# Kernel optimization log

Measured on AMD Instinct MI355X. Metric: run time of the kernel, lower is better.

## Reference

```python
import jax, jax.numpy as jnp
import numpy as np

B, S = 32, 2048
DIM_ACTION = 32
DIM_STRUCT = 64
HIDDEN = 128  # mlp_hidden_dim default = dim_action * 4
EPS = 1e-12   # F.normalize eps


def l2norm(t):
    n = jnp.linalg.norm(t, axis=-1, keepdims=True)
    return t / jnp.maximum(n, EPS)


def setup_inputs() -> dict:
    key = jax.random.key(0)
    ks = jax.random.split(key, 9)
    sd = lambda fan_in: 1.0 / np.sqrt(fan_in)
    inp = {
        "actions": jax.random.normal(ks[0], (B, S, DIM_ACTION), dtype=jnp.float32),
        # MLP: dim_action -> hidden -> hidden -> dim_structure^2 (depth=2 hidden relu layers)
        "w0": jax.random.uniform(ks[1], (DIM_ACTION, HIDDEN), jnp.float32, -sd(DIM_ACTION), sd(DIM_ACTION)),
        "b0": jnp.zeros((HIDDEN,), jnp.float32),
        "w1": jax.random.uniform(ks[2], (HIDDEN, HIDDEN), jnp.float32, -sd(HIDDEN), sd(HIDDEN)),
        "b1": jnp.zeros((HIDDEN,), jnp.float32),
        "w2": jax.random.uniform(ks[3], (HIDDEN, DIM_STRUCT * DIM_STRUCT), jnp.float32, -sd(HIDDEN), sd(HIDDEN)),
        "b2": jnp.zeros((DIM_STRUCT * DIM_STRUCT,), jnp.float32),
        # RNN init hidden parameter [1, dim_structure], ~N(0, 0.01)
        "init_hidden": jax.random.normal(ks[4], (1, DIM_STRUCT), dtype=jnp.float32) * 0.01,
    }
    return inp


def reference(actions, w0, b0, w1, b1, w2, b2, init_hidden):
    # MLP to transitions: [B, S, d*d]
    h = jax.nn.relu(jnp.einsum("bsa,ah->bsh", actions, w0) + b0)
    h = jax.nn.relu(jnp.einsum("bsh,hk->bsk", h, w1) + b1)
    t = jnp.einsum("bsh,ho->bso", h, w2) + b2
    transitions = t.reshape(B, S, DIM_STRUCT, DIM_STRUCT)  # [B, S, i, j]

    # RNN: hidden_{t+1} = l2norm(relu(hidden_t @ T_t)), scanned over seq
    hidden0 = jnp.broadcast_to(l2norm(init_hidden), (B, DIM_STRUCT))

    def step(hidden, trans):  # trans: [B, i, j]
        hidden = jnp.einsum("bi,bij->bj", hidden, trans)
        hidden = l2norm(jax.nn.relu(hidden))
        return hidden, hidden

    trans_seq = jnp.swapaxes(transitions, 0, 1)  # [S, B, i, j]
    _, hiddens = jax.lax.scan(step, hidden0, trans_seq)  # [S, B, d]
    return jnp.swapaxes(hiddens, 0, 1)  # [B, S, d]
```

## Files before the change

### kernel.cpp

```cpp
#include <hip/hip_runtime.h>

#define B_ 32
#define S_ 2048
#define DA 32
#define DH 128
#define DS 64
#define DS2 4096

typedef _Float16 half8 __attribute__((ext_vector_type(8)));
typedef float f32x4 __attribute__((ext_vector_type(4)));

template <int CTRL>
__device__ __forceinline__ float dpp_add(float x) {
  int t = __builtin_amdgcn_update_dpp(0, __float_as_int(x), CTRL, 0xF, 0xF, true);
  return x + __int_as_float(t);
}
__device__ __forceinline__ float row_sum16(float x) {
  x = dpp_add<0xB1>(x);
  x = dpp_add<0x4E>(x);
  x = dpp_add<0x141>(x);
  x = dpp_add<0x140>(x);
  return x;
}

__device__ __forceinline__ void gl2lds16(const void* g, void* l) {
  __builtin_amdgcn_global_load_lds(
      (const __attribute__((address_space(1))) void*)g,
      (__attribute__((address_space(3))) void*)l, 16, 0, 0);
}

struct SharedRnn {
  float4 ring[6][16][64];
  int flags[6];
  int cons;
};
struct SharedGemm {
  _Float16 Ah[128 * 128];
  _Float16 Al[128 * 128];
  _Float16 Bh[128 * 128];
  _Float16 Bl[128 * 128];
};
struct SharedMlp {
  float a_t[DA][64];
  float w0_l[DA][DH];
  float h0t[DH][64];
};
union SharedU {
  SharedRnn r;
  SharedGemm g;
  SharedMlp m;
};

__global__ __launch_bounds__(256) void k_split(
    const float* __restrict__ w2, _Float16* __restrict__ w2h,
    _Float16* __restrict__ w2l)
{
  for (int e = blockIdx.x * 256 + threadIdx.x; e < DH * DS2;
       e += gridDim.x * 256) {
    int n = e >> 7, k = e & 127;
    float v = w2[(size_t)k * DS2 + n];
    _Float16 hi = (_Float16)v;
    _Float16 lo = (_Float16)((v - (float)hi) * 2048.0f);
    int kk = k ^ ((n & 7) << 3);
    w2h[(size_t)n * DH + kk] = hi;
    w2l[(size_t)n * DH + kk] = lo;
  }
}

__device__ __forceinline__ void mlp_tile(
    const float* __restrict__ actions, const float* __restrict__ w0,
    const float* __restrict__ b0, const float* __restrict__ w1,
    const float* __restrict__ b1, _Float16* __restrict__ h1h,
    _Float16* __restrict__ h1l, int s_base, int m0, SharedMlp& sm, int tid)
{
#pragma unroll
  for (int q = 0; q < 2; ++q) {
    int g = tid + 256 * q;
    int tok = g >> 3, kq = g & 7;
    int tl = m0 + tok;
    int b = tl & 31, s = s_base + (tl >> 5);
    float4 v = *(const float4*)(actions + ((size_t)b * S_ + s) * DA + 4 * kq);
    sm.a_t[4 * kq + 0][tok] = v.x; sm.a_t[4 * kq + 1][tok] = v.y;
    sm.a_t[4 * kq + 2][tok] = v.z; sm.a_t[4 * kq + 3][tok] = v.w;
  }
#pragma unroll
  for (int q = 0; q < 4; ++q) {
    int g = tid + 256 * q;
    ((float4*)&sm.w0_l[0][0])[g] = ((const float4*)w0)[g];
  }
  __syncthreads();

  const int tm = tid & 15;
  const int tn = tid >> 4;

  float acc[4][8];
#pragma unroll
  for (int mi = 0; mi < 4; ++mi)
#pragma unroll
    for (int ni = 0; ni < 8; ++ni) acc[mi][ni] = 0.f;

#pragma unroll 4
  for (int k = 0; k < DA; ++k) {
    float4 a4 = *(const float4*)&sm.a_t[k][4 * tm];
    float4 wa = *(const float4*)&sm.w0_l[k][8 * tn];
    float4 wb = *(const float4*)&sm.w0_l[k][8 * tn + 4];
    float av[4] = {a4.x, a4.y, a4.z, a4.w};
    float wv[8] = {wa.x, wa.y, wa.z, wa.w, wb.x, wb.y, wb.z, wb.w};
#pragma unroll
    for (int mi = 0; mi < 4; ++mi)
#pragma unroll
      for (int ni = 0; ni < 8; ++ni) acc[mi][ni] += av[mi] * wv[ni];
  }
  {
    float4 ba = *(const float4*)(b0 + 8 * tn);
    float4 bb = *(const float4*)(b0 + 8 * tn + 4);
    float bv[8] = {ba.x, ba.y, ba.z, ba.w, bb.x, bb.y, bb.z, bb.w};
#pragma unroll
    for (int mi = 0; mi < 4; ++mi)
#pragma unroll
      for (int ni = 0; ni < 8; ++ni)
        sm.h0t[8 * tn + ni][4 * tm + mi] = fmaxf(acc[mi][ni] + bv[ni], 0.f);
  }
  __syncthreads();

  float acc1[4][8];
#pragma unroll
  for (int mi = 0; mi < 4; ++mi)
#pragma unroll
    for (int ni = 0; ni < 8; ++ni) acc1[mi][ni] = 0.f;

#pragma unroll 4
  for (int k = 0; k < DH; ++k) {
    float4 h4 = *(const float4*)&sm.h0t[k][4 * tm];
    float4 wa = *(const float4*)(w1 + (size_t)k * DH + 8 * tn);
    float4 wb = *(const float4*)(w1 + (size_t)k * DH + 8 * tn + 4);
    float av[4] = {h4.x, h4.y, h4.z, h4.w};
    float wv[8] = {wa.x, wa.y, wa.z, wa.w, wb.x, wb.y, wb.z, wb.w};
#pragma unroll
    for (int mi = 0; mi < 4; ++mi)
#pragma unroll
      for (int ni = 0; ni < 8; ++ni) acc1[mi][ni] += av[mi] * wv[ni];
  }
  {
    float4 ba = *(const float4*)(b1 + 8 * tn);
    float4 bb = *(const float4*)(b1 + 8 * tn + 4);
    float bv[8] = {ba.x, ba.y, ba.z, ba.w, bb.x, bb.y, bb.z, bb.w};
#pragma unroll
    for (int mi = 0; mi < 4; ++mi) {
      const int m = m0 + 4 * tm + mi;
      half8 hv, lv;
#pragma unroll
      for (int ni = 0; ni < 8; ++ni) {
        float h = fmaxf(acc1[mi][ni] + bv[ni], 0.f);
        _Float16 hi = (_Float16)h;
        hv[ni] = hi;
        lv[ni] = (_Float16)((h - (float)hi) * 2048.0f);
      }
      const int off = m * DH + ((8 * tn) ^ ((m & 7) << 3));
      *(half8*)(h1h + off) = hv;
      *(half8*)(h1l + off) = lv;
    }
  }
}

__device__ __forceinline__ void trans_loop(
    const _Float16* __restrict__ h1h, const _Float16* __restrict__ h1l,
    const _Float16* __restrict__ w2h, const _Float16* __restrict__ w2l,
    const float* __restrict__ b2, float* __restrict__ trans,
    int MT, int x, SharedGemm& sg, int tid)
{
  const int w  = tid >> 6;
  const int lw = tid & 63;
  const int strip = x / 7;
  const int idx   = x % 7;
  const int n0 = strip * 128;

  auto stage32k = [&](const _Float16* src, _Float16* dst) {
    const _Float16* s = src + w * 4096 + lw * 8;
    _Float16* d = dst + w * 4096;
#pragma unroll
    for (int i = 0; i < 8; ++i)
      gl2lds16(s + i * 512, d + i * 512);
  };

  stage32k(w2h + (size_t)n0 * DH, sg.Bh);
  stage32k(w2l + (size_t)n0 * DH, sg.Bl);

  const int fr = lw & 15;
  const int kg = lw >> 4;
  const int wr = w >> 1, wc = w & 1;

  float b2v[4];
#pragma unroll
  for (int fn = 0; fn < 4; ++fn)
    b2v[fn] = b2[n0 + wc * 64 + fn * 16 + fr];

  const f32x4 fz = {0.f, 0.f, 0.f, 0.f};

  for (int mt = idx; mt < MT; mt += 7) {
    const int m0 = mt * 128;
    stage32k(h1h + (size_t)m0 * DH, sg.Ah);
    stage32k(h1l + (size_t)m0 * DH, sg.Al);
    asm volatile("s_waitcnt vmcnt(0)" ::: "memory");
    __syncthreads();

    f32x4 ahh[4][4], axx[4][4], all_[4][4];
#pragma unroll
    for (int fm = 0; fm < 4; ++fm)
#pragma unroll
      for (int fn = 0; fn < 4; ++fn) {
        ahh[fm][fn] = fz;
        axx[fm][fn] = fz;
        all_[fm][fn] = fz;
      }

#pragma unroll
    for (int kc = 0; kc < 4; ++kc) {
      const int k0 = kc * 32 + kg * 8;
      half8 bh[4], bl[4];
#pragma unroll
      for (int fn = 0; fn < 4; ++fn) {
        const int n = wc * 64 + fn * 16 + fr;
        const int off = n * DH + (k0 ^ ((n & 7) << 3));
        bh[fn] = *(const half8*)&sg.Bh[off];
        bl[fn] = *(const half8*)&sg.Bl[off];
      }
#pragma unroll
      for (int fm = 0; fm < 4; ++fm) {
        const int m = wr * 64 + fm * 16 + fr;
        const int off = m * DH + (k0 ^ ((m & 7) << 3));
        half8 ah = *(const half8*)&sg.Ah[off];
        half8 al = *(const half8*)&sg.Al[off];
#pragma unroll
        for (int fn = 0; fn < 4; ++fn) {
          ahh[fm][fn] = __builtin_amdgcn_mfma_f32_16x16x32_f16(
              ah, bh[fn], ahh[fm][fn], 0, 0, 0);
          axx[fm][fn] = __builtin_amdgcn_mfma_f32_16x16x32_f16(
              ah, bl[fn], axx[fm][fn], 0, 0, 0);
          axx[fm][fn] = __builtin_amdgcn_mfma_f32_16x16x32_f16(
              al, bh[fn], axx[fm][fn], 0, 0, 0);
          all_[fm][fn] = __builtin_amdgcn_mfma_f32_16x16x32_f16(
              al, bl[fn], all_[fm][fn], 0, 0, 0);
        }
      }
    }
    __syncthreads();

#pragma unroll
    for (int fm = 0; fm < 4; ++fm) {
#pragma unroll
      for (int fn = 0; fn < 4; ++fn) {
        const int col = n0 + wc * 64 + fn * 16 + fr;
        float* dst = trans +
            (size_t)(m0 + wr * 64 + fm * 16 + kg * 4) * DS2 + col;
#pragma unroll
        for (int r = 0; r < 4; ++r) {
          float v = ahh[fm][fn][r] + axx[fm][fn][r] * (1.0f / 2048.0f) +
                    all_[fm][fn][r] * (1.0f / 4194304.0f) + b2v[fn];
          dst[(size_t)r * DS2] = v;
        }
      }
    }
  }
}

__global__ __launch_bounds__(256) void k_mlp01(
    const float* __restrict__ actions, const float* __restrict__ w0,
    const float* __restrict__ b0, const float* __restrict__ w1,
    const float* __restrict__ b1, _Float16* __restrict__ h1h,
    _Float16* __restrict__ h1l, int s_base)
{
  __shared__ SharedMlp sm;
  mlp_tile(actions, w0, b0, w1, b1, h1h, h1l, s_base, blockIdx.x * 64, sm,
           threadIdx.x);
}

__global__ __launch_bounds__(256, 1) void k_comb(
    const float* __restrict__ actions, const float* __restrict__ w0,
    const float* __restrict__ b0, const float* __restrict__ w1,
    const float* __restrict__ b1, const _Float16* __restrict__ w2h,
    const _Float16* __restrict__ w2l, const float* __restrict__ b2,
    const float* __restrict__ init_hidden,
    float* __restrict__ trans0, float* __restrict__ trans1,
    _Float16* __restrict__ h1h0, _Float16* __restrict__ h1l0,
    _Float16* __restrict__ h1h1, _Float16* __restrict__ h1l1,
    float* __restrict__ hstate, float* __restrict__ out,
    int c, int SC, int nch)
{
  __shared__ SharedU sh;
  const int tid = threadIdx.x;
  const int M = SC * 32;

  if (blockIdx.x >= 32) {
    const int x = blockIdx.x - 32;
    if (c < nch) {
      const _Float16* h1h = (c & 1) ? h1h1 : h1h0;
      const _Float16* h1l = (c & 1) ? h1l1 : h1l0;
      float* trans = (c & 1) ? trans1 : trans0;
      trans_loop(h1h, h1l, w2h, w2l, b2, trans, M / 128, x, sh.g, tid);
      if (c + 1 < nch) {
        __syncthreads();
        _Float16* hh = ((c + 1) & 1) ? h1h1 : h1h0;
        _Float16* hl = ((c + 1) & 1) ? h1l1 : h1l0;
        for (int j = x; j < M / 64; j += 224) {
          mlp_tile(actions, w0, b0, w1, b1, hh, hl, (c + 1) * SC, j * 64,
                   sh.m, tid);
          __syncthreads();
        }
      }
    }
    return;
  }

  if (c == 0) return;
  const int cc = c - 1;
  const float* trans = (cc & 1) ? trans1 : trans0;
  const int s_base = cc * SC;
  const int wv = tid >> 6;
  const int lane = tid & 63;
  const int b = blockIdx.x;

  if (tid < 6) sh.r.flags[tid] = 0;
  if (tid == 6) sh.r.cons = 0;
  __syncthreads();

  const float* base = trans + (size_t)b * DS2;

  if (wv > 0) {
    const int p = wv - 1;
    int prev = -1;
    for (int s = p; s < SC; s += 3) {
      while (s - __hip_atomic_load(&sh.r.cons, __ATOMIC_RELAXED,
                                   __HIP_MEMORY_SCOPE_WORKGROUP) > 5)
        __builtin_amdgcn_s_sleep(2);
      const int slot = s % 6;
      const float* g = base + (size_t)s * (32 * DS2) + 4 * lane;
      float* l = (float*)&sh.r.ring[slot][0][0];
#pragma unroll
      for (int q = 0; q < 16; ++q)
        gl2lds16(g + q * 256, l + q * 256);
      if (prev >= 0) {
        asm volatile("s_waitcnt vmcnt(16)" ::: "memory");
        __hip_atomic_store(&sh.r.flags[prev % 6], prev + 1, __ATOMIC_RELAXED,
                           __HIP_MEMORY_SCOPE_WORKGROUP);
      }
      prev = s;
    }
    if (prev >= 0) {
      asm volatile("s_waitcnt vmcnt(0)" ::: "memory");
      __hip_atomic_store(&sh.r.flags[prev % 6], prev + 1, __ATOMIC_RELAXED,
                         __HIP_MEMORY_SCOPE_WORKGROUP);
    }
  } else {
    const int d = lane >> 4;
    const int cq = lane & 15;
    const bool d1 = (d & 1), d2 = (d & 2);
    const int pb = lane & 48;

    float4 hq;
    if (cc == 0) {
      hq = *(const float4*)(init_hidden + 4 * cq);
      float ss0 = row_sum16(hq.x * hq.x + hq.y * hq.y + hq.z * hq.z + hq.w * hq.w);
      float iv0 = 1.0f / fmaxf(sqrtf(ss0), 1e-12f);
      hq.x *= iv0; hq.y *= iv0; hq.z *= iv0; hq.w *= iv0;
    } else {
      hq = *(const float4*)(hstate + b * DS + 4 * cq);
    }
    float inv_prev = 1.0f;

    float* outp = out + ((size_t)b * S_ + s_base) * DS + 4 * cq;
    int fpre = -1;
    for (int s = 0; s < SC; ++s) {
      const int slot = s % 6;
      if (fpre < s + 1) {
        while (__hip_atomic_load(&sh.r.flags[slot], __ATOMIC_ACQUIRE,
                                 __HIP_MEMORY_SCOPE_WORKGROUP) < s + 1)
          __builtin_amdgcn_s_sleep(0);
      }
      fpre = __hip_atomic_load(&sh.r.flags[(s + 1) % 6], __ATOMIC_ACQUIRE,
                               __HIP_MEMORY_SCOPE_WORKGROUP);

      float hsel = d2 ? (d1 ? hq.w : hq.z) : (d1 ? hq.y : hq.x);
      float ax = 0.f, ay = 0.f, az = 0.f, aw = 0.f;
#pragma unroll
      for (int q = 0; q < 16; ++q) {
        float4 t4 = sh.r.ring[slot][q][lane];
        float hb = __shfl(hsel, pb + q, 64);
        ax += hb * t4.x; ay += hb * t4.y;
        az += hb * t4.z; aw += hb * t4.w;
      }
      __hip_atomic_store(&sh.r.cons, s + 1, __ATOMIC_RELAXED,
                         __HIP_MEMORY_SCOPE_WORKGROUP);

      ax += __shfl_xor(ax, 16, 64); ax += __shfl_xor(ax, 32, 64);
      ay += __shfl_xor(ay, 16, 64); ay += __shfl_xor(ay, 32, 64);
      az += __shfl_xor(az, 16, 64); az += __shfl_xor(az, 32, 64);
      aw += __shfl_xor(aw, 16, 64); aw += __shfl_xor(aw, 32, 64);
      hq.x = fmaxf(ax * inv_prev, 0.f);
      hq.y = fmaxf(ay * inv_prev, 0.f);
      hq.z = fmaxf(az * inv_prev, 0.f);
      hq.w = fmaxf(aw * inv_prev, 0.f);
      float ss = row_sum16(hq.x * hq.x + hq.y * hq.y + hq.z * hq.z + hq.w * hq.w);
      float inv = 1.0f / fmaxf(sqrtf(ss), 1e-12f);
      if (d == 0) {
        float4 o;
        o.x = hq.x * inv; o.y = hq.y * inv; o.z = hq.z * inv; o.w = hq.w * inv;
        *(float4*)(outp + (size_t)s * DS) = o;
      }
      inv_prev = inv;
    }
    if (d == 0) {
      float4 o;
      o.x = hq.x * inv_prev; o.y = hq.y * inv_prev;
      o.z = hq.z * inv_prev; o.w = hq.w * inv_prev;
      *(float4*)(hstate + b * DS + 4 * cq) = o;
    }
  }
}

extern "C" void kernel_launch(void* const* d_in, const int* in_sizes, int n_in,
                              void* d_out, int out_size, void* d_ws, size_t ws_size,
                              hipStream_t stream) {
  const float* actions     = (const float*)d_in[0];
  const float* w0          = (const float*)d_in[1];
  const float* b0          = (const float*)d_in[2];
  const float* w1          = (const float*)d_in[3];
  const float* b1          = (const float*)d_in[4];
  const float* w2          = (const float*)d_in[5];
  const float* b2          = (const float*)d_in[6];
  const float* init_hidden = (const float*)d_in[7];
  float* out = (float*)d_out;

  int SC = 2048;
  while (SC > 4) {
    size_t need = 2 * (size_t)SC * 32 * DS2 * 4
                + 4 * (size_t)SC * 32 * DH * 2
                + 2 * (size_t)DH * DS2 * 2
                + (size_t)B_ * DS * 4;
    if (need <= ws_size) break;
    SC >>= 1;
  }
  char* p = (char*)d_ws;
  float* trans0 = (float*)p;        p += (size_t)SC * 32 * DS2 * 4;
  float* trans1 = (float*)p;        p += (size_t)SC * 32 * DS2 * 4;
  _Float16* h1h0 = (_Float16*)p;    p += (size_t)SC * 32 * DH * 2;
  _Float16* h1l0 = (_Float16*)p;    p += (size_t)SC * 32 * DH * 2;
  _Float16* h1h1 = (_Float16*)p;    p += (size_t)SC * 32 * DH * 2;
  _Float16* h1l1 = (_Float16*)p;    p += (size_t)SC * 32 * DH * 2;
  _Float16* w2h  = (_Float16*)p;    p += (size_t)DH * DS2 * 2;
  _Float16* w2l  = (_Float16*)p;    p += (size_t)DH * DS2 * 2;
  float* hstate  = (float*)p;

  const int M = SC * 32;
  const int nch = S_ / SC;

  hipLaunchKernelGGL(k_split, dim3(512), dim3(256), 0, stream, w2, w2h, w2l);
  hipLaunchKernelGGL(k_mlp01, dim3(M / 64), dim3(256), 0, stream,
                     actions, w0, b0, w1, b1, h1h0, h1l0, 0);
  for (int c = 0; c <= nch; ++c) {
    hipLaunchKernelGGL(k_comb, dim3(256), dim3(256), 0, stream,
                       actions, w0, b0, w1, b1, w2h, w2l, b2, init_hidden,
                       trans0, trans1, h1h0, h1l0, h1h1, h1l1, hstate, out,
                       c, SC, nch);
  }
}
```

Measured before the change: 1.584 ms.

## Store transition matrices as fp16 plus e4m3 residual to cut memory traffic

```diff
diff --git a/kernel.cpp b/kernel.cpp
--- a/kernel.cpp
+++ b/kernel.cpp
@@ -8,6 +8,7 @@
 #define DS2 4096
 
 typedef _Float16 half8 __attribute__((ext_vector_type(8)));
+typedef _Float16 half4v __attribute__((ext_vector_type(4)));
 typedef float f32x4 __attribute__((ext_vector_type(4)));
 
 template <int CTRL>
@@ -29,8 +30,34 @@
       (__attribute__((address_space(3))) void*)l, 16, 0, 0);
 }
 
+__device__ __forceinline__ unsigned f32_to_e4m3(float x) {
+  unsigned u = __float_as_uint(x);
+  unsigned s = (u >> 24) & 0x80u;
+  float ax = fabsf(x);
+  if (ax >= 448.f) return s | 0x7Eu;
+  if (ax < 0x1p-6f) {
+    int m = (int)rintf(ax * 512.f);
+    return s | (unsigned)m;
+  }
+  unsigned au = __float_as_uint(ax);
+  au += 0x7FFFFu + ((au >> 20) & 1u);
+  int e = (int)((au >> 23) & 0xffu) - 120;
+  if (e >= 16) return s | 0x7Eu;
+  unsigned m = (au >> 20) & 7u;
+  return s | ((unsigned)e << 3) | m;
+}
+
+__device__ __forceinline__ float e4m3_to_f32(unsigned b) {
+  unsigned e = (b >> 3) & 15u, m = b & 7u;
+  float vn = __uint_as_float(((e + 120u) << 23) | (m << 20));
+  float vs = (float)(int)m * 0x1p-9f;
+  float mag = e ? vn : vs;
+  return (b & 0x80u) ? -mag : mag;
+}
+
 struct SharedRnn {
-  float4 ring[6][16][64];
+  _Float16 ringh[6][4096];
+  unsigned char ringl[6][4096];
   int flags[6];
   int cons;
 };
@@ -166,7 +193,8 @@
 __device__ __forceinline__ void trans_loop(
     const _Float16* __restrict__ h1h, const _Float16* __restrict__ h1l,
     const _Float16* __restrict__ w2h, const _Float16* __restrict__ w2l,
-    const float* __restrict__ b2, float* __restrict__ trans,
+    const float* __restrict__ b2, _Float16* __restrict__ transh,
+    unsigned char* __restrict__ translo,
     int MT, int x, SharedGemm& sg, int tid)
 {
   const int w  = tid >> 6;
@@ -251,13 +279,17 @@
 #pragma unroll
       for (int fn = 0; fn < 4; ++fn) {
         const int col = n0 + wc * 64 + fn * 16 + fr;
-        float* dst = trans +
-            (size_t)(m0 + wr * 64 + fm * 16 + kg * 4) * DS2 + col;
+        const size_t rowb = (size_t)(m0 + wr * 64 + fm * 16 + kg * 4);
+        _Float16* dsth = transh + rowb * DS2 + col;
+        unsigned char* dstl = translo + rowb * DS2 + col;
 #pragma unroll
         for (int r = 0; r < 4; ++r) {
           float v = ahh[fm][fn][r] + axx[fm][fn][r] * (1.0f / 2048.0f) +
                     all_[fm][fn][r] * (1.0f / 4194304.0f) + b2v[fn];
-          dst[(size_t)r * DS2] = v;
+          _Float16 hi = (_Float16)v;
+          dsth[(size_t)r * DS2] = hi;
+          float res = (v - (float)hi) * 2048.0f;
+          dstl[(size_t)r * DS2] = (unsigned char)f32_to_e4m3(res);
         }
       }
     }
@@ -281,7 +313,8 @@
     const float* __restrict__ b1, const _Float16* __restrict__ w2h,
     const _Float16* __restrict__ w2l, const float* __restrict__ b2,
     const float* __restrict__ init_hidden,
-    float* __restrict__ trans0, float* __restrict__ trans1,
+    _Float16* __restrict__ transh0, _Float16* __restrict__ transh1,
+    unsigned char* __restrict__ translo0, unsigned char* __restrict__ translo1,
     _Float16* __restrict__ h1h0, _Float16* __restrict__ h1l0,
     _Float16* __restrict__ h1h1, _Float16* __restrict__ h1l1,
     float* __restrict__ hstate, float* __restrict__ out,
@@ -296,8 +329,10 @@
     if (c < nch) {
       const _Float16* h1h = (c & 1) ? h1h1 : h1h0;
       const _Float16* h1l = (c & 1) ? h1l1 : h1l0;
-      float* trans = (c & 1) ? trans1 : trans0;
-      trans_loop(h1h, h1l, w2h, w2l, b2, trans, M / 128, x, sh.g, tid);
+      _Float16* transh = (c & 1) ? transh1 : transh0;
+      unsigned char* translo = (c & 1) ? translo1 : translo0;
+      trans_loop(h1h, h1l, w2h, w2l, b2, transh, translo, M / 128, x, sh.g,
+                 tid);
       if (c + 1 < nch) {
         __syncthreads();
         _Float16* hh = ((c + 1) & 1) ? h1h1 : h1h0;
@@ -314,7 +349,8 @@
 
   if (c == 0) return;
   const int cc = c - 1;
-  const float* trans = (cc & 1) ? trans1 : trans0;
+  const _Float16* transh = (cc & 1) ? transh1 : transh0;
+  const unsigned char* translo = (cc & 1) ? translo1 : translo0;
   const int s_base = cc * SC;
   const int wv = tid >> 6;
   const int lane = tid & 63;
@@ -324,7 +360,8 @@
   if (tid == 6) sh.r.cons = 0;
   __syncthreads();
 
-  const float* base = trans + (size_t)b * DS2;
+  const _Float16* baseh = transh + (size_t)b * DS2;
+  const unsigned char* basel = translo + (size_t)b * DS2;
 
   if (wv > 0) {
     const int p = wv - 1;
@@ -334,13 +371,18 @@
                                    __HIP_MEMORY_SCOPE_WORKGROUP) > 5)
         __builtin_amdgcn_s_sleep(2);
       const int slot = s % 6;
-      const float* g = base + (size_t)s * (32 * DS2) + 4 * lane;
-      float* l = (float*)&sh.r.ring[slot][0][0];
-#pragma unroll
-      for (int q = 0; q < 16; ++q)
-        gl2lds16(g + q * 256, l + q * 256);
+      const _Float16* gh = baseh + (size_t)s * (32 * DS2) + 8 * lane;
+      _Float16* lh = &sh.r.ringh[slot][0];
+#pragma unroll
+      for (int q = 0; q < 8; ++q)
+        gl2lds16(gh + q * 512, lh + q * 512);
+      const unsigned char* gl = basel + (size_t)s * (32 * DS2) + 16 * lane;
+      unsigned char* ll = &sh.r.ringl[slot][0];
+#pragma unroll
+      for (int q = 0; q < 4; ++q)
+        gl2lds16(gl + q * 1024, ll + q * 1024);
       if (prev >= 0) {
-        asm volatile("s_waitcnt vmcnt(16)" ::: "memory");
+        asm volatile("s_waitcnt vmcnt(12)" ::: "memory");
         __hip_atomic_store(&sh.r.flags[prev % 6], prev + 1, __ATOMIC_RELAXED,
                            __HIP_MEMORY_SCOPE_WORKGROUP);
       }
@@ -356,6 +398,7 @@
     const int cq = lane & 15;
     const bool d1 = (d & 1), d2 = (d & 2);
     const int pb = lane & 48;
+    const int off0 = 64 * d + 4 * cq;
 
     float4 hq;
     if (cc == 0) {
@@ -384,10 +427,16 @@
       float ax = 0.f, ay = 0.f, az = 0.f, aw = 0.f;
 #pragma unroll
       for (int q = 0; q < 16; ++q) {
-        float4 t4 = sh.r.ring[slot][q][lane];
+        const int eo = off0 + 256 * q;
+        half4v t4 = *(const half4v*)&sh.r.ringh[slot][eo];
+        unsigned l4 = *(const unsigned*)&sh.r.ringl[slot][eo];
         float hb = __shfl(hsel, pb + q, 64);
-        ax += hb * t4.x; ay += hb * t4.y;
-        az += hb * t4.z; aw += hb * t4.w;
+        float v0 = fmaf(e4m3_to_f32(l4 & 0xffu), (1.0f / 2048.0f), (float)t4[0]);
+        float v1 = fmaf(e4m3_to_f32((l4 >> 8) & 0xffu), (1.0f / 2048.0f), (float)t4[1]);
+        float v2 = fmaf(e4m3_to_f32((l4 >> 16) & 0xffu), (1.0f / 2048.0f), (float)t4[2]);
+        float v3 = fmaf(e4m3_to_f32(l4 >> 24), (1.0f / 2048.0f), (float)t4[3]);
+        ax += hb * v0; ay += hb * v1;
+        az += hb * v2; aw += hb * v3;
       }
       __hip_atomic_store(&sh.r.cons, s + 1, __ATOMIC_RELAXED,
                          __HIP_MEMORY_SCOPE_WORKGROUP);
@@ -433,7 +482,8 @@
 
   int SC = 2048;
   while (SC > 4) {
-    size_t need = 2 * (size_t)SC * 32 * DS2 * 4
+    size_t need = 2 * (size_t)SC * 32 * DS2 * 2
+                + 2 * (size_t)SC * 32 * DS2
                 + 4 * (size_t)SC * 32 * DH * 2
                 + 2 * (size_t)DH * DS2 * 2
                 + (size_t)B_ * DS * 4;
@@ -441,14 +491,16 @@
     SC >>= 1;
   }
   char* p = (char*)d_ws;
-  float* trans0 = (float*)p;        p += (size_t)SC * 32 * DS2 * 4;
-  float* trans1 = (float*)p;        p += (size_t)SC * 32 * DS2 * 4;
-  _Float16* h1h0 = (_Float16*)p;    p += (size_t)SC * 32 * DH * 2;
-  _Float16* h1l0 = (_Float16*)p;    p += (size_t)SC * 32 * DH * 2;
-  _Float16* h1h1 = (_Float16*)p;    p += (size_t)SC * 32 * DH * 2;
-  _Float16* h1l1 = (_Float16*)p;    p += (size_t)SC * 32 * DH * 2;
-  _Float16* w2h  = (_Float16*)p;    p += (size_t)DH * DS2 * 2;
-  _Float16* w2l  = (_Float16*)p;    p += (size_t)DH * DS2 * 2;
+  _Float16* transh0 = (_Float16*)p;      p += (size_t)SC * 32 * DS2 * 2;
+  _Float16* transh1 = (_Float16*)p;      p += (size_t)SC * 32 * DS2 * 2;
+  _Float16* h1h0 = (_Float16*)p;         p += (size_t)SC * 32 * DH * 2;
+  _Float16* h1l0 = (_Float16*)p;         p += (size_t)SC * 32 * DH * 2;
+  _Float16* h1h1 = (_Float16*)p;         p += (size_t)SC * 32 * DH * 2;
+  _Float16* h1l1 = (_Float16*)p;         p += (size_t)SC * 32 * DH * 2;
+  _Float16* w2h  = (_Float16*)p;         p += (size_t)DH * DS2 * 2;
+  _Float16* w2l  = (_Float16*)p;         p += (size_t)DH * DS2 * 2;
+  unsigned char* translo0 = (unsigned char*)p;  p += (size_t)SC * 32 * DS2;
+  unsigned char* translo1 = (unsigned char*)p;  p += (size_t)SC * 32 * DS2;
   float* hstate  = (float*)p;
 
   const int M = SC * 32;
@@ -460,7 +512,8 @@
   for (int c = 0; c <= nch; ++c) {
     hipLaunchKernelGGL(k_comb, dim3(256), dim3(256), 0, stream,
                        actions, w0, b0, w1, b1, w2h, w2l, b2, init_hidden,
-                       trans0, trans1, h1h0, h1l0, h1h1, h1l1, hstate, out,
+                       transh0, transh1, translo0, translo1,
+                       h1h0, h1l0, h1h1, h1l1, hstate, out,
                        c, SC, nch);
   }
 }
```

Measured after the change: 4.814 ms. 3.04x slower.

## Give each RNN lane one output column and double-buffer transitions in registers

Applied to the files above, without the earlier changes.

```diff
diff --git a/kernel.cpp b/kernel.cpp
--- a/kernel.cpp
+++ b/kernel.cpp
@@ -31,6 +31,7 @@
 
 struct SharedRnn {
   float4 ring[6][16][64];
+  float hlds[64];
   int flags[6];
   int cons;
 };
@@ -352,69 +353,83 @@
                          __HIP_MEMORY_SCOPE_WORKGROUP);
     }
   } else {
-    const int d = lane >> 4;
-    const int cq = lane & 15;
-    const bool d1 = (d & 1), d2 = (d & 2);
-    const int pb = lane & 48;
-
-    float4 hq;
+    float h[64];
+    float TA[64], TB[64];
+    float inv_prev = 1.0f;
+    float hj;
+
     if (cc == 0) {
-      hq = *(const float4*)(init_hidden + 4 * cq);
-      float ss0 = row_sum16(hq.x * hq.x + hq.y * hq.y + hq.z * hq.z + hq.w * hq.w);
-      float iv0 = 1.0f / fmaxf(sqrtf(ss0), 1e-12f);
-      hq.x *= iv0; hq.y *= iv0; hq.z *= iv0; hq.w *= iv0;
+      float v = init_hidden[lane];
+      float t0 = v * v;
+      t0 = row_sum16(t0);
+      t0 += __shfl_xor(t0, 16, 64);
+      t0 += __shfl_xor(t0, 32, 64);
+      float iv0 = 1.0f / fmaxf(sqrtf(t0), 1e-12f);
+      hj = v * iv0;
     } else {
-      hq = *(const float4*)(hstate + b * DS + 4 * cq);
-    }
-    float inv_prev = 1.0f;
-
-    float* outp = out + ((size_t)b * S_ + s_base) * DS + 4 * cq;
-    int fpre = -1;
-    for (int s = 0; s < SC; ++s) {
-      const int slot = s % 6;
-      if (fpre < s + 1) {
-        while (__hip_atomic_load(&sh.r.flags[slot], __ATOMIC_ACQUIRE,
-                                 __HIP_MEMORY_SCOPE_WORKGROUP) < s + 1)
+      hj = hstate[b * DS + lane];
+    }
+    sh.r.hlds[lane] = hj;
+#pragma unroll
+    for (int g = 0; g < 16; ++g) {
+      float4 v4 = *(const float4*)&sh.r.hlds[4 * g];
+      h[4 * g] = v4.x; h[4 * g + 1] = v4.y;
+      h[4 * g + 2] = v4.z; h[4 * g + 3] = v4.w;
+    }
+
+    float* outp = out + ((size_t)b * S_ + s_base) * DS + lane;
+    const float* ringf = (const float*)&sh.r.ring[0][0][0];
+
+    while (__hip_atomic_load(&sh.r.flags[0], __ATOMIC_ACQUIRE,
+                             __HIP_MEMORY_SCOPE_WORKGROUP) < 1)
+      __builtin_amdgcn_s_sleep(0);
+#pragma unroll
+    for (int i = 0; i < 64; ++i) TA[i] = ringf[i * 64 + lane];
+
+    auto step_body = [&](float (&Tc)[64], float (&Tn)[64], int s) {
+      if (s + 1 < SC) {
+        const int sl = (s + 1) % 6;
+        while (__hip_atomic_load(&sh.r.flags[sl], __ATOMIC_ACQUIRE,
+                                 __HIP_MEMORY_SCOPE_WORKGROUP) < s + 2)
           __builtin_amdgcn_s_sleep(0);
-      }
-      fpre = __hip_atomic_load(&sh.r.flags[(s + 1) % 6], __ATOMIC_ACQUIRE,
-                               __HIP_MEMORY_SCOPE_WORKGROUP);
-
-      float hsel = d2 ? (d1 ? hq.w : hq.z) : (d1 ? hq.y : hq.x);
-      float ax = 0.f, ay = 0.f, az = 0.f, aw = 0.f;
-#pragma unroll
-      for (int q = 0; q < 16; ++q) {
-        float4 t4 = sh.r.ring[slot][q][lane];
-        float hb = __shfl(hsel, pb + q, 64);
-        ax += hb * t4.x; ay += hb * t4.y;
-        az += hb * t4.z; aw += hb * t4.w;
+        const float* rp = ringf + sl * 4096;
+#pragma unroll
+        for (int i = 0; i < 64; ++i) Tn[i] = rp[i * 64 + lane];
+      }
+      float a0 = 0.f, a1 = 0.f, a2 = 0.f, a3 = 0.f;
+#pragma unroll
+      for (int i = 0; i < 64; i += 4) {
+        a0 = fmaf(h[i], Tc[i], a0);
+        a1 = fmaf(h[i + 1], Tc[i + 1], a1);
+        a2 = fmaf(h[i + 2], Tc[i + 2], a2);
+        a3 = fmaf(h[i + 3], Tc[i + 3], a3);
       }
       __hip_atomic_store(&sh.r.cons, s + 1, __ATOMIC_RELAXED,
                          __HIP_MEMORY_SCOPE_WORKGROUP);
-
-      ax += __shfl_xor(ax, 16, 64); ax += __shfl_xor(ax, 32, 64);
-      ay += __shfl_xor(ay, 16, 64); ay += __shfl_xor(ay, 32, 64);
-      az += __shfl_xor(az, 16, 64); az += __shfl_xor(az, 32, 64);
-      aw += __shfl_xor(aw, 16, 64); aw += __shfl_xor(aw, 32, 64);
-      hq.x = fmaxf(ax * inv_prev, 0.f);
-      hq.y = fmaxf(ay * inv_prev, 0.f);
-      hq.z = fmaxf(az * inv_prev, 0.f);
-      hq.w = fmaxf(aw * inv_prev, 0.f);
-      float ss = row_sum16(hq.x * hq.x + hq.y * hq.y + hq.z * hq.z + hq.w * hq.w);
-      float inv = 1.0f / fmaxf(sqrtf(ss), 1e-12f);
-      if (d == 0) {
-        float4 o;
-        o.x = hq.x * inv; o.y = hq.y * inv; o.z = hq.z * inv; o.w = hq.w * inv;
-        *(float4*)(outp + (size_t)s * DS) = o;
+      float ax = (a0 + a1) + (a2 + a3);
+      hj = fmaxf(ax * inv_prev, 0.f);
+      float t = hj * hj;
+      t = row_sum16(t);
+      t += __shfl_xor(t, 16, 64);
+      t += __shfl_xor(t, 32, 64);
+      float inv = 1.0f / fmaxf(sqrtf(t), 1e-12f);
+      outp[(size_t)s * DS] = hj * inv;
+      sh.r.hlds[lane] = hj;
+#pragma unroll
+      for (int g = 0; g < 16; ++g) {
+        float4 v4 = *(const float4*)&sh.r.hlds[4 * g];
+        h[4 * g] = v4.x; h[4 * g + 1] = v4.y;
+        h[4 * g + 2] = v4.z; h[4 * g + 3] = v4.w;
       }
       inv_prev = inv;
-    }
-    if (d == 0) {
-      float4 o;
-      o.x = hq.x * inv_prev; o.y = hq.y * inv_prev;
-      o.z = hq.z * inv_prev; o.w = hq.w * inv_prev;
-      *(float4*)(hstate + b * DS + 4 * cq) = o;
-    }
+    };
+
+    for (int s = 0; s < SC; s += 2) {
+      step_body(TA, TB, s);
+      step_body(TB, TA, s + 1);
+    }
+
+    hstate[b * DS + lane] = hj * inv_prev;
   }
 }
 
```

Result: slower. 1.659 ms (+4.7%).
